# Kernel optimization log

Measured on AMD Instinct MI355X. Metric: run time of the kernel, lower is better.

Reference implementation:

```python
import jax, jax.numpy as jnp
import numpy as np

N_NODES = 50000
N_EDGES = 800000
IN_DIM = 256
NHID = 64
OUT_DIM = 64
DEPTH = 4
P = 2.0


def _gcn_conv(x, W, b, src, dst, n):
    # PyG GCNConv: xW, add self-loops, sym-normalize, aggregate src->dst, + bias
    xw = x @ W
    loop = jnp.arange(n)
    s = jnp.concatenate([src, loop])
    d = jnp.concatenate([dst, loop])
    deg = jax.ops.segment_sum(jnp.ones_like(d, dtype=xw.dtype), d, num_segments=n)
    dis = jnp.where(deg > 0, jax.lax.rsqrt(jnp.maximum(deg, 1.0)), 0.0)
    w = dis[s] * dis[d]  # [E+n]
    out = jax.ops.segment_sum(w[:, None] * xw[s], d, num_segments=n)
    return out + b


def _g2_gate(x, W, b, src, dst, n):
    xg = jax.nn.relu(_gcn_conv(x, W, b, src, dst, n))
    diff = jnp.abs(xg[src] - xg[dst]) ** P  # [E, nhid]
    sums = jax.ops.segment_sum(diff, src, num_segments=n)
    cnt = jax.ops.segment_sum(jnp.ones((src.shape[0],), dtype=x.dtype), src, num_segments=n)
    return jnp.tanh(sums / jnp.maximum(cnt, 1.0)[:, None])


def setup_inputs() -> dict:
    key = jax.random.key(0)
    ks = jax.random.split(key, 10)
    x = jax.random.normal(ks[0], (N_NODES, IN_DIM), dtype=jnp.float32)
    edge_index = jax.random.randint(ks[1], (2, N_EDGES), 0, N_NODES, dtype=jnp.int64 if jax.config.jax_enable_x64 else jnp.int32)
    s = 0.05
    return {
        "x": x,
        "edge_index": edge_index,
        "enc_w": jax.random.normal(ks[2], (IN_DIM, NHID), dtype=jnp.float32) * s,
        "enc_b": jnp.zeros((NHID,), dtype=jnp.float32),
        "conv_w": jax.random.normal(ks[3], (NHID, NHID), dtype=jnp.float32) * s,
        "conv_b": jnp.zeros((NHID,), dtype=jnp.float32),
        "gg_w": jax.random.normal(ks[4], (NHID, NHID), dtype=jnp.float32) * s,
        "gg_b": jnp.zeros((NHID,), dtype=jnp.float32),
        "dec_w": jax.random.normal(ks[5], (NHID, OUT_DIM), dtype=jnp.float32) * s,
        "dec_b": jnp.zeros((OUT_DIM,), dtype=jnp.float32),
    }


def reference(x, edge_index, enc_w, enc_b, conv_w, conv_b, gg_w, gg_b, dec_w, dec_b):
    n = x.shape[0]
    src, dst = edge_index[0], edge_index[1]
    # eval mode: dropouts are identity
    X = jax.nn.relu(x @ enc_w + enc_b)
    for _ in range(DEPTH):
        X_ = jax.nn.relu(_gcn_conv(X, conv_w, conv_b, src, dst, n))
        tau = _g2_gate(X, gg_w, gg_b, src, dst, n)
        X = (1.0 - tau) * X + tau * X_
    X = jax.nn.relu(X @ dec_w + dec_b)
    return X
```

## Files before the change

kernel.cpp:

```cpp
#include <hip/hip_runtime.h>
#include <math.h>

#define NN 50000
#define NE 800000
#define IND 256
#define NH 64
#define DEPTH 4
#define PART_DIV 6250
#define SB 49
#define EPP 100000


__device__ __forceinline__ unsigned short f2bf(float f) {
    unsigned int x = __float_as_uint(f);
    unsigned int r = (x + 0x7fffu + ((x >> 16) & 1u)) >> 16;
    return (unsigned short)r;
}
__device__ __forceinline__ unsigned int pack2bf(float lo, float hi) {
    return (unsigned int)f2bf(lo) | ((unsigned int)f2bf(hi) << 16);
}
__device__ __forceinline__ ushort4 f4_to_us4(float4 f) {
    ushort4 u;
    u.x = f2bf(f.x); u.y = f2bf(f.y); u.z = f2bf(f.z); u.w = f2bf(f.w);
    return u;
}
__device__ __forceinline__ void acc8(float* a, uint4 r) {
    a[0] += __uint_as_float(r.x << 16); a[1] += __uint_as_float(r.x & 0xffff0000u);
    a[2] += __uint_as_float(r.y << 16); a[3] += __uint_as_float(r.y & 0xffff0000u);
    a[4] += __uint_as_float(r.z << 16); a[5] += __uint_as_float(r.z & 0xffff0000u);
    a[6] += __uint_as_float(r.w << 16); a[7] += __uint_as_float(r.w & 0xffff0000u);
}
__device__ __forceinline__ void unpack8(float* a, uint4 r) {
    a[0] = __uint_as_float(r.x << 16); a[1] = __uint_as_float(r.x & 0xffff0000u);
    a[2] = __uint_as_float(r.y << 16); a[3] = __uint_as_float(r.y & 0xffff0000u);
    a[4] = __uint_as_float(r.z << 16); a[5] = __uint_as_float(r.z & 0xffff0000u);
    a[6] = __uint_as_float(r.w << 16); a[7] = __uint_as_float(r.w & 0xffff0000u);
}
__device__ __forceinline__ void accd8(float* a, const float* xg, uint4 r) {
    float e;
    e = xg[0] - __uint_as_float(r.x << 16);         a[0] += e * e;
    e = xg[1] - __uint_as_float(r.x & 0xffff0000u); a[1] += e * e;
    e = xg[2] - __uint_as_float(r.y << 16);         a[2] += e * e;
    e = xg[3] - __uint_as_float(r.y & 0xffff0000u); a[3] += e * e;
    e = xg[4] - __uint_as_float(r.z << 16);         a[4] += e * e;
    e = xg[5] - __uint_as_float(r.z & 0xffff0000u); a[5] += e * e;
    e = xg[6] - __uint_as_float(r.w << 16);         a[6] += e * e;
    e = xg[7] - __uint_as_float(r.w & 0xffff0000u); a[7] += e * e;
}
__device__ __forceinline__ float tanh_pos(float x) {
    float t = __expf(-2.f * x);
    return (1.f - t) / (1.f + t);
}


__global__ void count8(const int* __restrict__ src, const int* __restrict__ dst,
                       int* __restrict__ hin, int* __restrict__ hout,
                       int* __restrict__ lrin, int* __restrict__ lrout,
                       int nGroups) {
    int p = blockIdx.x & 7;
    int g = blockIdx.x >> 3;
    int* hi = hin + p * NN;
    int* ho = hout + p * NN;
    for (int i = g * 256 + threadIdx.x; i < EPP; i += nGroups * 256) {
        int e = p * EPP + i;
        int s = src[e], d = dst[e];
        lrin[e]  = atomicAdd(&hi[d], 1);
        lrout[e] = atomicAdd(&ho[s], 1);
    }
}

__global__ void reduce8(int* __restrict__ hin, int* __restrict__ hout,
                        int* __restrict__ degin, int* __restrict__ degout) {
    int i = blockIdx.x * blockDim.x + threadIdx.x;
    if (i >= NN) return;
    int run = 0;
#pragma unroll
    for (int p = 0; p < 8; ++p) {
        int t = hin[p * NN + i]; hin[p * NN + i] = run; run += t;
    }
    degin[i] = run;
    run = 0;
#pragma unroll
    for (int p = 0; p < 8; ++p) {
        int t = hout[p * NN + i]; hout[p * NN + i] = run; run += t;
    }
    degout[i] = run;
}

__global__ __launch_bounds__(512) void scan_p1(const int* __restrict__ in0,
                                               const int* __restrict__ in1,
                                               int* __restrict__ tmp,
                                               int* __restrict__ bsum) {
    int a = blockIdx.x / SB;
    int b = blockIdx.x % SB;
    const int* in = a ? in1 : in0;
    int t = threadIdx.x;
    int base = b * 1024 + t * 2;
    int v0 = (base < NN) ? in[base] : 0;
    int v1 = (base + 1 < NN) ? in[base + 1] : 0;
    int v = v0 + v1;
    int x = v;
#pragma unroll
    for (int off = 1; off < 64; off <<= 1) {
        int u = __shfl_up(x, off);
        if ((t & 63) >= off) x += u;
    }
    __shared__ int ws[8];
    int wid = t >> 6, lane = t & 63;
    if (lane == 63) ws[wid] = x;
    __syncthreads();
    if (t == 0) {
        int run = 0;
#pragma unroll
        for (int w = 0; w < 8; ++w) { int s = ws[w]; ws[w] = run; run += s; }
    }
    __syncthreads();
    x += ws[wid];
    int excl = x - v;
    if (base < NN) tmp[a * NN + base] = excl;
    if (base + 1 < NN) tmp[a * NN + base + 1] = excl + v0;
    if (t == 511) bsum[a * SB + b] = x;
}

__global__ __launch_bounds__(128) void scan_p2(int* __restrict__ bsum,
                                               int* __restrict__ out0,
                                               int* __restrict__ out1) {
    int t = threadIdx.x;
    int a = t >> 6, lane = t & 63;
    int v = (lane < SB) ? bsum[a * SB + lane] : 0;
    int x = v;
#pragma unroll
    for (int off = 1; off < 64; off <<= 1) {
        int u = __shfl_up(x, off);
        if (lane >= off) x += u;
    }
    if (lane < SB) bsum[a * SB + lane] = x - v;
    if (lane == SB - 1) {
        if (a == 0) out0[NN] = x; else out1[NN] = x;
    }
}

__global__ __launch_bounds__(512) void scan_p3(const int* __restrict__ tmp,
                                               const int* __restrict__ bsum,
                                               int* __restrict__ out0,
                                               int* __restrict__ out1) {
    int a = blockIdx.x / SB;
    int b = blockIdx.x % SB;
    int* out = a ? out1 : out0;
    int add = bsum[a * SB + b];
    int t = threadIdx.x;
    int base = b * 1024 + t * 2;
    if (base < NN) out[base] = tmp[a * NN + base] + add;
    if (base + 1 < NN) out[base + 1] = tmp[a * NN + base + 1] + add;
}

__global__ void init_node(const int* __restrict__ degin, const int* __restrict__ degout,
                          float* __restrict__ dis, float* __restrict__ cntf) {
    int i = blockIdx.x * blockDim.x + threadIdx.x;
    if (i < NN) {
        dis[i] = rsqrtf((float)(degin[i] + 1));
        int od = degout[i];
        cntf[i] = (float)(od > 0 ? od : 1);
    }
}

__global__ void fill_csr_part(const int* __restrict__ src, const int* __restrict__ dst,
                              const int* __restrict__ off_dst, const int* __restrict__ off_src,
                              const int* __restrict__ hin, const int* __restrict__ hout,
                              const int* __restrict__ lrin, const int* __restrict__ lrout,
                              int* __restrict__ srcs_by_dst, int* __restrict__ dsts_by_src,
                              int nGroups) {
    int q = blockIdx.x & 7;
    int g = blockIdx.x >> 3;
    for (int pe = 0; pe < 8; ++pe) {
        const int* bin = hin + pe * NN;
        const int* bout = hout + pe * NN;
        for (int i = g * 256 + threadIdx.x; i < EPP; i += nGroups * 256) {
            int e = pe * EPP + i;
            int s = src[e], d = dst[e];
            if (d / PART_DIV == q) srcs_by_dst[off_dst[d] + bin[d] + lrin[e]] = s;
            if (s / PART_DIV == q) dsts_by_src[off_src[s] + bout[s] + lrout[e]] = d;
        }
    }
}

__global__ void bucket_hist(const int* __restrict__ degin, const int* __restrict__ degout,
                            int* __restrict__ ghin, int* __restrict__ ghout) {
    __shared__ int lin[128], lout[128];
    int t = threadIdx.x;
    if (t < 128) { lin[t] = 0; lout[t] = 0; }
    __syncthreads();
    int i = blockIdx.x * 256 + t;
    if (i < NN) {
        atomicAdd(&lin[min(degin[i], 127)], 1);
        atomicAdd(&lout[min(degout[i], 127)], 1);
    }
    __syncthreads();
    if (t < 128) {
        if (lin[t])  atomicAdd(&ghin[t],  lin[t]);
        if (lout[t]) atomicAdd(&ghout[t], lout[t]);
    }
}

__global__ void bucket_scan(const int* __restrict__ ghin, const int* __restrict__ ghout,
                            int* __restrict__ curin, int* __restrict__ curout) {
    __shared__ int a[128], b[128];
    int t = threadIdx.x;
    if (t < 128) a[t] = ghin[t]; else b[t - 128] = ghout[t - 128];
    __syncthreads();
    if (t == 0) { int run = 0; for (int k = 0; k < 128; ++k) { int v = a[k]; a[k] = run; run += v; } }
    if (t == 1) { int run = 0; for (int k = 0; k < 128; ++k) { int v = b[k]; b[k] = run; run += v; } }
    __syncthreads();
    if (t < 128) curin[t] = a[t]; else curout[t - 128] = b[t - 128];
}

__global__ void bucket_scatter(const int* __restrict__ degin, const int* __restrict__ degout,
                               int* __restrict__ curin, int* __restrict__ curout,
                               int* __restrict__ order_in, int* __restrict__ order_out) {
    __shared__ int lin[128], lout[128], basein[128], baseout[128];
    int t = threadIdx.x;
    if (t < 128) { lin[t] = 0; lout[t] = 0; }
    __syncthreads();
    int i = blockIdx.x * 256 + t;
    int bi = 0, bo = 0, ri = 0, ro = 0;
    if (i < NN) {
        bi = min(degin[i], 127);  ri = atomicAdd(&lin[bi], 1);
        bo = min(degout[i], 127); ro = atomicAdd(&lout[bo], 1);
    }
    __syncthreads();
    if (t < 128) {
        basein[t]  = lin[t]  ? atomicAdd(&curin[t],  lin[t])  : 0;
        baseout[t] = lout[t] ? atomicAdd(&curout[t], lout[t]) : 0;
    }
    __syncthreads();
    if (i < NN) {
        order_in[basein[bi] + ri] = i;
        order_out[baseout[bo] + ro] = i;
    }
}

template<int K, bool RELU, bool WSC>
__global__ __launch_bounds__(256) void gemm64b(const float* __restrict__ X,
                                               const float* __restrict__ W,
                                               const float* __restrict__ bias,
                                               const float* __restrict__ rowscale,
                                               float* __restrict__ out,
                                               unsigned short* __restrict__ xsc, int n) {
    __shared__ float Ws[64 * 64];
    __shared__ float Xs[64][68];
    int tid = threadIdx.x;
    int row0 = blockIdx.x * 64;
    int r16 = tid >> 4;
    int cg = tid & 15;
    float4 acc[4];
#pragma unroll
    for (int t = 0; t < 4; ++t) acc[t] = make_float4(0.f, 0.f, 0.f, 0.f);

    for (int kc = 0; kc < K; kc += 64) {
        const float4* W4 = (const float4*)(W + (size_t)kc * 64);
        float4* Ws4 = (float4*)Ws;
#pragma unroll
        for (int t = 0; t < 4; ++t) Ws4[tid + t * 256] = W4[tid + t * 256];
#pragma unroll
        for (int t = 0; t < 4; ++t) {
            int r = r16 + t * 16;
            int grow = row0 + r;
            float4 xv = make_float4(0.f, 0.f, 0.f, 0.f);
            if (grow < n) xv = *(const float4*)(X + (size_t)grow * K + kc + cg * 4);
            Xs[r][cg * 4 + 0] = xv.x; Xs[r][cg * 4 + 1] = xv.y;
            Xs[r][cg * 4 + 2] = xv.z; Xs[r][cg * 4 + 3] = xv.w;
        }
        __syncthreads();
#pragma unroll
        for (int k = 0; k < 64; ++k) {
            float4 w4 = ((const float4*)Ws)[k * 16 + cg];
#pragma unroll
            for (int t = 0; t < 4; ++t) {
                float xv = Xs[r16 + t * 16][k];
                acc[t].x += xv * w4.x; acc[t].y += xv * w4.y;
                acc[t].z += xv * w4.z; acc[t].w += xv * w4.w;
            }
        }
        __syncthreads();
    }

    float4 b4 = ((const float4*)bias)[cg];
#pragma unroll
    for (int t = 0; t < 4; ++t) {
        int row = row0 + r16 + t * 16;
        if (row < n) {
            float4 o;
            o.x = acc[t].x + b4.x; o.y = acc[t].y + b4.y;
            o.z = acc[t].z + b4.z; o.w = acc[t].w + b4.w;
            if (RELU) {
                o.x = fmaxf(o.x, 0.f); o.y = fmaxf(o.y, 0.f);
                o.z = fmaxf(o.z, 0.f); o.w = fmaxf(o.w, 0.f);
            }
            ((float4*)(out + (size_t)row * 64))[cg] = o;
            if (WSC) {
                float s = rowscale[row];
                float4 o2 = make_float4(o.x * s, o.y * s, o.z * s, o.w * s);
                ((ushort4*)(xsc + (size_t)row * 64))[cg] = f4_to_us4(o2);
            }
        }
    }
}

__global__ __launch_bounds__(256) void dualgemm32(
    const float* __restrict__ Z,
    const float* __restrict__ Wb, const float* __restrict__ bb,
    const float* __restrict__ Wc, const float* __restrict__ bc,
    unsigned short* __restrict__ Bbf, unsigned short* __restrict__ Cbf, int n)
{
    __shared__ float W2[64 * 128];
    __shared__ float Xs[32][68];
    int tid = threadIdx.x;
    int row0 = blockIdx.x * 32;
    {
        const float4* wb4 = (const float4*)Wb;
        const float4* wc4 = (const float4*)Wc;
#pragma unroll
        for (int t = 0; t < 4; ++t) {
            int idx = tid + t * 256;
            int k = idx >> 4, c = (idx & 15) * 4;
            *(float4*)&W2[k * 128 + c]      = wb4[idx];
            *(float4*)&W2[k * 128 + 64 + c] = wc4[idx];
        }
#pragma unroll
        for (int t = 0; t < 2; ++t) {
            int idx = tid + t * 256;
            int r = idx >> 4, c4 = idx & 15;
            int gr = row0 + r;
            float4 xv = make_float4(0.f, 0.f, 0.f, 0.f);
            if (gr < n) xv = *(const float4*)(Z + (size_t)gr * 64 + c4 * 4);
            Xs[r][c4 * 4 + 0] = xv.x; Xs[r][c4 * 4 + 1] = xv.y;
            Xs[r][c4 * 4 + 2] = xv.z; Xs[r][c4 * 4 + 3] = xv.w;
        }
    }
    __syncthreads();

    int r8 = tid >> 5;
    int cg = tid & 31;
    float4 acc[4];
#pragma unroll
    for (int t = 0; t < 4; ++t) acc[t] = make_float4(0.f, 0.f, 0.f, 0.f);
#pragma unroll
    for (int k = 0; k < 64; ++k) {
        float4 w4 = *(const float4*)&W2[k * 128 + cg * 4];
#pragma unroll
        for (int t = 0; t < 4; ++t) {
            float xv = Xs[r8 + t * 8][k];
            acc[t].x += xv * w4.x; acc[t].y += xv * w4.y;
            acc[t].z += xv * w4.z; acc[t].w += xv * w4.w;
        }
    }

    float4 bv = (cg < 16) ? ((const float4*)bb)[cg] : ((const float4*)bc)[cg - 16];
#pragma unroll
    for (int t = 0; t < 4; ++t) {
        int row = row0 + r8 + t * 8;
        if (row < n) {
            float4 o;
            o.x = fmaxf(acc[t].x + bv.x, 0.f); o.y = fmaxf(acc[t].y + bv.y, 0.f);
            o.z = fmaxf(acc[t].z + bv.z, 0.f); o.w = fmaxf(acc[t].w + bv.w, 0.f);
            if (cg < 16) ((ushort4*)(Bbf + (size_t)row * 64))[cg]      = f4_to_us4(o);
            else         ((ushort4*)(Cbf + (size_t)row * 64))[cg - 16] = f4_to_us4(o);
        }
    }
}

__global__ __launch_bounds__(256) void zgather(
    const unsigned short* __restrict__ Xbf,
    const int* __restrict__ off, const int* __restrict__ nbr,
    const float* __restrict__ dis, const int* __restrict__ order,
    float* __restrict__ Z)
{
    int t = blockIdx.x * 256 + threadIdx.x;
    int idx = t >> 3, l8 = t & 7;
    if (idx >= NN) return;
    int node = order[idx];
    const uint4* Xb = (const uint4*)Xbf;
    float a[8];
    unpack8(a, Xb[(size_t)node * 8 + l8]);
    int lo = off[node], hi = off[node + 1];
    int j = lo;
    for (; j + 7 < hi; j += 8) {
        int s0 = nbr[j],     s1 = nbr[j + 1], s2 = nbr[j + 2], s3 = nbr[j + 3];
        int s4 = nbr[j + 4], s5 = nbr[j + 5], s6 = nbr[j + 6], s7 = nbr[j + 7];
        uint4 r0 = Xb[(size_t)s0 * 8 + l8];
        uint4 r1 = Xb[(size_t)s1 * 8 + l8];
        uint4 r2 = Xb[(size_t)s2 * 8 + l8];
        uint4 r3 = Xb[(size_t)s3 * 8 + l8];
        uint4 r4 = Xb[(size_t)s4 * 8 + l8];
        uint4 r5 = Xb[(size_t)s5 * 8 + l8];
        uint4 r6 = Xb[(size_t)s6 * 8 + l8];
        uint4 r7 = Xb[(size_t)s7 * 8 + l8];
        acc8(a, r0); acc8(a, r1); acc8(a, r2); acc8(a, r3);
        acc8(a, r4); acc8(a, r5); acc8(a, r6); acc8(a, r7);
    }
    for (; j + 3 < hi; j += 4) {
        int s0 = nbr[j], s1 = nbr[j + 1], s2 = nbr[j + 2], s3 = nbr[j + 3];
        uint4 r0 = Xb[(size_t)s0 * 8 + l8];
        uint4 r1 = Xb[(size_t)s1 * 8 + l8];
        uint4 r2 = Xb[(size_t)s2 * 8 + l8];
        uint4 r3 = Xb[(size_t)s3 * 8 + l8];
        acc8(a, r0); acc8(a, r1); acc8(a, r2); acc8(a, r3);
    }
    for (; j < hi; ++j) {
        acc8(a, Xb[(size_t)nbr[j] * 8 + l8]);
    }
    float di = dis[node];
    float* zp = Z + (size_t)node * 64 + l8 * 8;
    *(float4*)(zp)     = make_float4(di * a[0], di * a[1], di * a[2], di * a[3]);
    *(float4*)(zp + 4) = make_float4(di * a[4], di * a[5], di * a[6], di * a[7]);
}

__global__ __launch_bounds__(256) void gate_update8(
    const unsigned short* __restrict__ Cbf, const unsigned short* __restrict__ Xnbf,
    float* __restrict__ X, unsigned short* __restrict__ Xbf,
    const int* __restrict__ off, const int* __restrict__ nbr,
    const float* __restrict__ cntf, const float* __restrict__ dis,
    const int* __restrict__ order)
{
    int t = blockIdx.x * 256 + threadIdx.x;
    int idx = t >> 3, l8 = t & 7;
    if (idx >= NN) return;
    int node = order[idx];
    const uint4* Cb = (const uint4*)Cbf;
    float xg[8];
    unpack8(xg, Cb[(size_t)node * 8 + l8]);
    float a[8] = {0.f, 0.f, 0.f, 0.f, 0.f, 0.f, 0.f, 0.f};
    int lo = off[node], hi = off[node + 1];
    int j = lo;
    for (; j + 7 < hi; j += 8) {
        int d0 = nbr[j],     d1 = nbr[j + 1], d2 = nbr[j + 2], d3 = nbr[j + 3];
        int d4 = nbr[j + 4], d5 = nbr[j + 5], d6 = nbr[j + 6], d7 = nbr[j + 7];
        uint4 r0 = Cb[(size_t)d0 * 8 + l8];
        uint4 r1 = Cb[(size_t)d1 * 8 + l8];
        uint4 r2 = Cb[(size_t)d2 * 8 + l8];
        uint4 r3 = Cb[(size_t)d3 * 8 + l8];
        uint4 r4 = Cb[(size_t)d4 * 8 + l8];
        uint4 r5 = Cb[(size_t)d5 * 8 + l8];
        uint4 r6 = Cb[(size_t)d6 * 8 + l8];
        uint4 r7 = Cb[(size_t)d7 * 8 + l8];
        accd8(a, xg, r0); accd8(a, xg, r1); accd8(a, xg, r2); accd8(a, xg, r3);
        accd8(a, xg, r4); accd8(a, xg, r5); accd8(a, xg, r6); accd8(a, xg, r7);
    }
    for (; j + 3 < hi; j += 4) {
        int d0 = nbr[j], d1 = nbr[j + 1], d2 = nbr[j + 2], d3 = nbr[j + 3];
        uint4 r0 = Cb[(size_t)d0 * 8 + l8];
        uint4 r1 = Cb[(size_t)d1 * 8 + l8];
        uint4 r2 = Cb[(size_t)d2 * 8 + l8];
        uint4 r3 = Cb[(size_t)d3 * 8 + l8];
        accd8(a, xg, r0); accd8(a, xg, r1); accd8(a, xg, r2); accd8(a, xg, r3);
    }
    for (; j < hi; ++j) {
        accd8(a, xg, Cb[(size_t)nbr[j] * 8 + l8]);
    }
    float inv = 1.f / cntf[node];
    float di = dis[node];
    float xn[8];
    unpack8(xn, ((const uint4*)Xnbf)[(size_t)node * 8 + l8]);
    const float* xop = X + (size_t)node * 64 + l8 * 8;
    float o[8];
#pragma unroll
    for (int k = 0; k < 8; ++k) {
        float tau = tanh_pos(a[k] * inv);
        float xo = xop[k];
        o[k] = xo + tau * (xn[k] - xo);
    }
    float* xp = X + (size_t)node * 64 + l8 * 8;
    *(float4*)(xp)     = make_float4(o[0], o[1], o[2], o[3]);
    *(float4*)(xp + 4) = make_float4(o[4], o[5], o[6], o[7]);
    uint4 pk;
    pk.x = pack2bf(o[0] * di, o[1] * di);
    pk.y = pack2bf(o[2] * di, o[3] * di);
    pk.z = pack2bf(o[4] * di, o[5] * di);
    pk.w = pack2bf(o[6] * di, o[7] * di);
    ((uint4*)Xbf)[(size_t)node * 8 + l8] = pk;
}


extern "C" void kernel_launch(void* const* d_in, const int* in_sizes, int n_in,
                              void* d_out, int out_size, void* d_ws, size_t ws_size,
                              hipStream_t stream) {
    const float* x      = (const float*)d_in[0];
    const int*   ei     = (const int*)d_in[1];
    const float* enc_w  = (const float*)d_in[2];
    const float* enc_b  = (const float*)d_in[3];
    const float* conv_w = (const float*)d_in[4];
    const float* conv_b = (const float*)d_in[5];
    const float* gg_w   = (const float*)d_in[6];
    const float* gg_b   = (const float*)d_in[7];
    const float* dec_w  = (const float*)d_in[8];
    const float* dec_b  = (const float*)d_in[9];
    float* out = (float*)d_out;

    const int* src = ei;
    const int* dst = ei + NE;

    char* p = (char*)d_ws;
    auto alloc = [&](size_t bytes) -> void* {
        void* r = (void*)p;
        p += (bytes + 255) & ~(size_t)255;
        return r;
    };
    float* X   = (float*)alloc((size_t)NN * 64 * 4);
    float* Zb  = (float*)alloc((size_t)NN * 64 * 4);
    unsigned short* Bbf = (unsigned short*)alloc((size_t)NN * 64 * 2);
    unsigned short* Xbf = (unsigned short*)alloc((size_t)NN * 64 * 2);
    unsigned short* Cbf = (unsigned short*)alloc((size_t)NN * 64 * 2);
    float* dis  = (float*)alloc((size_t)NN * 4);
    float* cntf = (float*)alloc((size_t)NN * 4);
    int* degin   = (int*)alloc((size_t)NN * 4);
    int* degout  = (int*)alloc((size_t)NN * 4);
    int* off_dst = (int*)alloc((size_t)(NN + 1) * 4);
    int* off_src = (int*)alloc((size_t)(NN + 1) * 4);
    int* hin     = (int*)alloc((size_t)8 * NN * 4);
    int* hout    = (int*)alloc((size_t)8 * NN * 4);
    int* lrin    = (int*)alloc((size_t)NE * 4);
    int* lrout   = (int*)alloc((size_t)NE * 4);
    int* sbd     = (int*)alloc((size_t)NE * 4);
    int* dbs     = (int*)alloc((size_t)NE * 4);
    int* stmp    = (int*)alloc((size_t)2 * NN * 4);
    int* bsum    = (int*)alloc((size_t)2 * SB * 4);
    int* order_in  = (int*)alloc((size_t)NN * 4);
    int* order_out = (int*)alloc((size_t)NN * 4);
    int* gbins   = (int*)alloc((size_t)512 * 4);
    int* ghin = gbins, *ghout = gbins + 128, *curin = gbins + 256, *curout = gbins + 384;

    hipMemsetAsync(hin, 0, (size_t)8 * NN * 4, stream);
    hipMemsetAsync(hout, 0, (size_t)8 * NN * 4, stream);
    hipMemsetAsync(gbins, 0, (size_t)512 * 4, stream);

    const int NB = (NN + 255) / 256;
    const int NGROUPS = 104;
    count8<<<8 * NGROUPS, 256, 0, stream>>>(src, dst, hin, hout, lrin, lrout, NGROUPS);
    reduce8<<<NB, 256, 0, stream>>>(hin, hout, degin, degout);
    scan_p1<<<2 * SB, 512, 0, stream>>>(degin, degout, stmp, bsum);
    scan_p2<<<1, 128, 0, stream>>>(bsum, off_dst, off_src);
    scan_p3<<<2 * SB, 512, 0, stream>>>(stmp, bsum, off_dst, off_src);
    init_node<<<NB, 256, 0, stream>>>(degin, degout, dis, cntf);
    bucket_hist<<<NB, 256, 0, stream>>>(degin, degout, ghin, ghout);
    bucket_scan<<<1, 256, 0, stream>>>(ghin, ghout, curin, curout);
    bucket_scatter<<<NB, 256, 0, stream>>>(degin, degout, curin, curout,
                                           order_in, order_out);
    fill_csr_part<<<8 * NGROUPS, 256, 0, stream>>>(src, dst, off_dst, off_src,
                                                   hin, hout, lrin, lrout,
                                                   sbd, dbs, NGROUPS);

    const int GB   = (NN + 63) / 64;
    const int GB32 = (NN + 31) / 32;
    const int OB   = ((NN * 8) + 255) / 256;

    gemm64b<IND, true, true><<<GB, 256, 0, stream>>>(x, enc_w, enc_b, dis, X, Xbf, NN);

    for (int l = 0; l < DEPTH; ++l) {
        zgather<<<OB, 256, 0, stream>>>(Xbf, off_dst, sbd, dis, order_in, Zb);
        dualgemm32<<<GB32, 256, 0, stream>>>(Zb, conv_w, conv_b, gg_w, gg_b, Bbf, Cbf, NN);
        gate_update8<<<OB, 256, 0, stream>>>(Cbf, Bbf, X, Xbf, off_src, dbs,
                                             cntf, dis, order_out);
    }

    gemm64b<NH, true, false><<<GB, 256, 0, stream>>>(X, dec_w, dec_b, nullptr, out, nullptr, NN);
}
```

Baseline: 651.8 us.

## Fuse degree counting with encoder GEMM and drop partitioned histograms

The 8-way partitioned per-node histograms and their reduce kernel are replaced by direct global atomics on degin/degout, with per-edge ranks taken from the atomic return. Counting blocks are interleaved with encoder GEMM blocks in one launch so the two independent workloads overlap. The bf16 scaled copy of X is produced in a separate init_pack kernel after dis is known. This removes one launch, the 8xNN histogram memsets and reads, and the reduce pass, at the cost of more atomic contention on shared counters and an extra pass over X.

Measured after the change: 625.7 us. 1.04x faster.

```diff
diff --git a/kernel.cpp b/kernel.cpp
--- a/kernel.cpp
+++ b/kernel.cpp
@@ -8,7 +8,7 @@
 #define DEPTH 4
 #define PART_DIV 6250
 #define SB 49
-#define EPP 100000
+#define CEB 782
 
 
 __device__ __forceinline__ unsigned short f2bf(float f) {
@@ -52,39 +52,71 @@
     return (1.f - t) / (1.f + t);
 }
 
-
-__global__ void count8(const int* __restrict__ src, const int* __restrict__ dst,
-                       int* __restrict__ hin, int* __restrict__ hout,
-                       int* __restrict__ lrin, int* __restrict__ lrout,
-                       int nGroups) {
-    int p = blockIdx.x & 7;
-    int g = blockIdx.x >> 3;
-    int* hi = hin + p * NN;
-    int* ho = hout + p * NN;
-    for (int i = g * 256 + threadIdx.x; i < EPP; i += nGroups * 256) {
-        int e = p * EPP + i;
-        int s = src[e], d = dst[e];
-        lrin[e]  = atomicAdd(&hi[d], 1);
-        lrout[e] = atomicAdd(&ho[s], 1);
-    }
-}
-
-__global__ void reduce8(int* __restrict__ hin, int* __restrict__ hout,
-                        int* __restrict__ degin, int* __restrict__ degout) {
-    int i = blockIdx.x * blockDim.x + threadIdx.x;
-    if (i >= NN) return;
-    int run = 0;
-#pragma unroll
-    for (int p = 0; p < 8; ++p) {
-        int t = hin[p * NN + i]; hin[p * NN + i] = run; run += t;
-    }
-    degin[i] = run;
-    run = 0;
-#pragma unroll
-    for (int p = 0; p < 8; ++p) {
-        int t = hout[p * NN + i]; hout[p * NN + i] = run; run += t;
-    }
-    degout[i] = run;
+__global__ __launch_bounds__(256) void count_enc(
+    const int* __restrict__ src, const int* __restrict__ dst,
+    int* __restrict__ degin, int* __restrict__ degout,
+    int* __restrict__ rank_in, int* __restrict__ rank_out,
+    const float* __restrict__ x, const float* __restrict__ enc_w,
+    const float* __restrict__ enc_b, float* __restrict__ X)
+{
+    __shared__ float Ws[64 * 64];
+    __shared__ float Xs[64][68];
+    int bid = blockIdx.x;
+    if ((bid & 1) == 0) {
+        int c = bid >> 1;
+        for (int e = c * 256 + threadIdx.x; e < NE; e += CEB * 256) {
+            int s = src[e], d = dst[e];
+            rank_in[e]  = atomicAdd(&degin[d], 1);
+            rank_out[e] = atomicAdd(&degout[s], 1);
+        }
+        return;
+    }
+    int tid = threadIdx.x;
+    int row0 = (bid >> 1) * 64;
+    int r16 = tid >> 4;
+    int cg = tid & 15;
+    float4 acc[4];
+#pragma unroll
+    for (int t = 0; t < 4; ++t) acc[t] = make_float4(0.f, 0.f, 0.f, 0.f);
+
+    for (int kc = 0; kc < IND; kc += 64) {
+        const float4* W4 = (const float4*)(enc_w + (size_t)kc * 64);
+        float4* Ws4 = (float4*)Ws;
+#pragma unroll
+        for (int t = 0; t < 4; ++t) Ws4[tid + t * 256] = W4[tid + t * 256];
+#pragma unroll
+        for (int t = 0; t < 4; ++t) {
+            int r = r16 + t * 16;
+            int grow = row0 + r;
+            float4 xv = make_float4(0.f, 0.f, 0.f, 0.f);
+            if (grow < NN) xv = *(const float4*)(x + (size_t)grow * IND + kc + cg * 4);
+            Xs[r][cg * 4 + 0] = xv.x; Xs[r][cg * 4 + 1] = xv.y;
+            Xs[r][cg * 4 + 2] = xv.z; Xs[r][cg * 4 + 3] = xv.w;
+        }
+        __syncthreads();
+#pragma unroll
+        for (int k = 0; k < 64; ++k) {
+            float4 w4 = ((const float4*)Ws)[k * 16 + cg];
+#pragma unroll
+            for (int t = 0; t < 4; ++t) {
+                float xv = Xs[r16 + t * 16][k];
+                acc[t].x += xv * w4.x; acc[t].y += xv * w4.y;
+                acc[t].z += xv * w4.z; acc[t].w += xv * w4.w;
+            }
+        }
+        __syncthreads();
+    }
+    float4 b4 = ((const float4*)enc_b)[cg];
+#pragma unroll
+    for (int t = 0; t < 4; ++t) {
+        int row = row0 + r16 + t * 16;
+        if (row < NN) {
+            float4 o;
+            o.x = fmaxf(acc[t].x + b4.x, 0.f); o.y = fmaxf(acc[t].y + b4.y, 0.f);
+            o.z = fmaxf(acc[t].z + b4.z, 0.f); o.w = fmaxf(acc[t].w + b4.w, 0.f);
+            ((float4*)(X + (size_t)row * 64))[cg] = o;
+        }
+    }
 }
 
 __global__ __launch_bounds__(512) void scan_p1(const int* __restrict__ in0,
@@ -154,34 +186,28 @@
     if (base + 1 < NN) out[base + 1] = tmp[a * NN + base + 1] + add;
 }
 
-__global__ void init_node(const int* __restrict__ degin, const int* __restrict__ degout,
-                          float* __restrict__ dis, float* __restrict__ cntf) {
-    int i = blockIdx.x * blockDim.x + threadIdx.x;
-    if (i < NN) {
-        dis[i] = rsqrtf((float)(degin[i] + 1));
-        int od = degout[i];
-        cntf[i] = (float)(od > 0 ? od : 1);
-    }
-}
-
-__global__ void fill_csr_part(const int* __restrict__ src, const int* __restrict__ dst,
-                              const int* __restrict__ off_dst, const int* __restrict__ off_src,
-                              const int* __restrict__ hin, const int* __restrict__ hout,
-                              const int* __restrict__ lrin, const int* __restrict__ lrout,
-                              int* __restrict__ srcs_by_dst, int* __restrict__ dsts_by_src,
-                              int nGroups) {
-    int q = blockIdx.x & 7;
-    int g = blockIdx.x >> 3;
-    for (int pe = 0; pe < 8; ++pe) {
-        const int* bin = hin + pe * NN;
-        const int* bout = hout + pe * NN;
-        for (int i = g * 256 + threadIdx.x; i < EPP; i += nGroups * 256) {
-            int e = pe * EPP + i;
-            int s = src[e], d = dst[e];
-            if (d / PART_DIV == q) srcs_by_dst[off_dst[d] + bin[d] + lrin[e]] = s;
-            if (s / PART_DIV == q) dsts_by_src[off_src[s] + bout[s] + lrout[e]] = d;
-        }
-    }
+__global__ __launch_bounds__(256) void init_pack(
+    const int* __restrict__ degin, const int* __restrict__ degout,
+    float* __restrict__ dis, float* __restrict__ cntf,
+    const float* __restrict__ X, unsigned short* __restrict__ Xbf)
+{
+    int t = blockIdx.x * 256 + threadIdx.x;
+    int node = t >> 3, l8 = t & 7;
+    if (node >= NN) return;
+    float di = rsqrtf((float)(degin[node] + 1));
+    if (l8 == 0) {
+        dis[node] = di;
+        int od = degout[node];
+        cntf[node] = (float)(od > 0 ? od : 1);
+    }
+    const float4* xp = (const float4*)(X + (size_t)node * 64 + l8 * 8);
+    float4 v0 = xp[0], v1 = xp[1];
+    uint4 pk;
+    pk.x = pack2bf(v0.x * di, v0.y * di);
+    pk.y = pack2bf(v0.z * di, v0.w * di);
+    pk.z = pack2bf(v1.x * di, v1.y * di);
+    pk.w = pack2bf(v1.z * di, v1.w * di);
+    ((uint4*)Xbf)[(size_t)node * 8 + l8] = pk;
 }
 
 __global__ void bucket_hist(const int* __restrict__ degin, const int* __restrict__ degout,
@@ -239,13 +265,25 @@
     }
 }
 
-template<int K, bool RELU, bool WSC>
+__global__ void fill_csr_part(const int* __restrict__ src, const int* __restrict__ dst,
+                              const int* __restrict__ off_dst, const int* __restrict__ off_src,
+                              const int* __restrict__ rank_in, const int* __restrict__ rank_out,
+                              int* __restrict__ srcs_by_dst, int* __restrict__ dsts_by_src,
+                              int nGroups) {
+    int q = blockIdx.x & 7;
+    int g = blockIdx.x >> 3;
+    for (int e = g * 256 + threadIdx.x; e < NE; e += nGroups * 256) {
+        int s = src[e], d = dst[e];
+        if (d / PART_DIV == q) srcs_by_dst[off_dst[d] + rank_in[e]] = s;
+        if (s / PART_DIV == q) dsts_by_src[off_src[s] + rank_out[e]] = d;
+    }
+}
+
+template<int K>
 __global__ __launch_bounds__(256) void gemm64b(const float* __restrict__ X,
                                                const float* __restrict__ W,
                                                const float* __restrict__ bias,
-                                               const float* __restrict__ rowscale,
-                                               float* __restrict__ out,
-                                               unsigned short* __restrict__ xsc, int n) {
+                                               float* __restrict__ out, int n) {
     __shared__ float Ws[64 * 64];
     __shared__ float Xs[64][68];
     int tid = threadIdx.x;
@@ -290,18 +328,9 @@
         int row = row0 + r16 + t * 16;
         if (row < n) {
             float4 o;
-            o.x = acc[t].x + b4.x; o.y = acc[t].y + b4.y;
-            o.z = acc[t].z + b4.z; o.w = acc[t].w + b4.w;
-            if (RELU) {
-                o.x = fmaxf(o.x, 0.f); o.y = fmaxf(o.y, 0.f);
-                o.z = fmaxf(o.z, 0.f); o.w = fmaxf(o.w, 0.f);
-            }
+            o.x = fmaxf(acc[t].x + b4.x, 0.f); o.y = fmaxf(acc[t].y + b4.y, 0.f);
+            o.z = fmaxf(acc[t].z + b4.z, 0.f); o.w = fmaxf(acc[t].w + b4.w, 0.f);
             ((float4*)(out + (size_t)row * 64))[cg] = o;
-            if (WSC) {
-                float s = rowscale[row];
-                float4 o2 = make_float4(o.x * s, o.y * s, o.z * s, o.w * s);
-                ((ushort4*)(xsc + (size_t)row * 64))[cg] = f4_to_us4(o2);
-            }
         }
     }
 }
@@ -516,10 +545,8 @@
     int* degout  = (int*)alloc((size_t)NN * 4);
     int* off_dst = (int*)alloc((size_t)(NN + 1) * 4);
     int* off_src = (int*)alloc((size_t)(NN + 1) * 4);
-    int* hin     = (int*)alloc((size_t)8 * NN * 4);
-    int* hout    = (int*)alloc((size_t)8 * NN * 4);
-    int* lrin    = (int*)alloc((size_t)NE * 4);
-    int* lrout   = (int*)alloc((size_t)NE * 4);
+    int* rank_in  = (int*)alloc((size_t)NE * 4);
+    int* rank_out = (int*)alloc((size_t)NE * 4);
     int* sbd     = (int*)alloc((size_t)NE * 4);
     int* dbs     = (int*)alloc((size_t)NE * 4);
     int* stmp    = (int*)alloc((size_t)2 * NN * 4);
@@ -529,31 +556,29 @@
     int* gbins   = (int*)alloc((size_t)512 * 4);
     int* ghin = gbins, *ghout = gbins + 128, *curin = gbins + 256, *curout = gbins + 384;
 
-    hipMemsetAsync(hin, 0, (size_t)8 * NN * 4, stream);
-    hipMemsetAsync(hout, 0, (size_t)8 * NN * 4, stream);
+    hipMemsetAsync(degin, 0, (size_t)NN * 4, stream);
+    hipMemsetAsync(degout, 0, (size_t)NN * 4, stream);
     hipMemsetAsync(gbins, 0, (size_t)512 * 4, stream);
 
     const int NB = (NN + 255) / 256;
+    const int OB = ((NN * 8) + 255) / 256;
     const int NGROUPS = 104;
-    count8<<<8 * NGROUPS, 256, 0, stream>>>(src, dst, hin, hout, lrin, lrout, NGROUPS);
-    reduce8<<<NB, 256, 0, stream>>>(hin, hout, degin, degout);
+
+    count_enc<<<2 * CEB, 256, 0, stream>>>(src, dst, degin, degout,
+                                           rank_in, rank_out, x, enc_w, enc_b, X);
     scan_p1<<<2 * SB, 512, 0, stream>>>(degin, degout, stmp, bsum);
     scan_p2<<<1, 128, 0, stream>>>(bsum, off_dst, off_src);
     scan_p3<<<2 * SB, 512, 0, stream>>>(stmp, bsum, off_dst, off_src);
-    init_node<<<NB, 256, 0, stream>>>(degin, degout, dis, cntf);
+    init_pack<<<OB, 256, 0, stream>>>(degin, degout, dis, cntf, X, Xbf);
     bucket_hist<<<NB, 256, 0, stream>>>(degin, degout, ghin, ghout);
     bucket_scan<<<1, 256, 0, stream>>>(ghin, ghout, curin, curout);
     bucket_scatter<<<NB, 256, 0, stream>>>(degin, degout, curin, curout,
                                            order_in, order_out);
     fill_csr_part<<<8 * NGROUPS, 256, 0, stream>>>(src, dst, off_dst, off_src,
-                                                   hin, hout, lrin, lrout,
-                                                   sbd, dbs, NGROUPS);
+                                                   rank_in, rank_out, sbd, dbs, NGROUPS);
 
     const int GB   = (NN + 63) / 64;
     const int GB32 = (NN + 31) / 32;
-    const int OB   = ((NN * 8) + 255) / 256;
-
-    gemm64b<IND, true, true><<<GB, 256, 0, stream>>>(x, enc_w, enc_b, dis, X, Xbf, NN);
 
     for (int l = 0; l < DEPTH; ++l) {
         zgather<<<OB, 256, 0, stream>>>(Xbf, off_dst, sbd, dis, order_in, Zb);
@@ -562,5 +587,5 @@
                                              cntf, dis, order_out);
     }
 
-    gemm64b<NH, true, false><<<GB, 256, 0, stream>>>(X, dec_w, dec_b, nullptr, out, nullptr, NN);
-}
+    gemm64b<NH><<<GB, 256, 0, stream>>>(X, dec_w, dec_b, out, NN);
+}
```
